# Kernel tuning notes

Measured on AMD Instinct MI355X. Metric: run time of the kernel, lower is better.

## Reference

```python
import jax, jax.numpy as jnp
import numpy as np
import math

T = 4096          # num tokens (== context_window_len)
IN_SIZE = 2048    # model dim
HEAD_SIZE = 128   # per-head dim


def setup_inputs() -> dict:
    key = jax.random.key(0)
    kx, kq, kk, kv = jax.random.split(key, 4)
    scale = 1.0 / math.sqrt(IN_SIZE)
    x = jax.random.normal(kx, (T, IN_SIZE), dtype=jnp.float32)
    # eqx.nn.Linear(in, out) weight has shape [out, in], applied as W @ x
    Wq = jax.random.normal(kq, (HEAD_SIZE, IN_SIZE), dtype=jnp.float32) * scale
    Wk = jax.random.normal(kk, (HEAD_SIZE, IN_SIZE), dtype=jnp.float32) * scale
    Wv = jax.random.normal(kv, (HEAD_SIZE, IN_SIZE), dtype=jnp.float32) * scale
    return {"x": x, "Wq": Wq, "Wk": Wk, "Wv": Wv}


def reference(x, Wq, Wk, Wv):
    # q, k, v: [T, head_size]
    q = x @ Wq.T
    k = x @ Wk.T
    v = x @ Wv.T
    # scores: [T, T]
    scores = (q @ k.T) / math.sqrt(HEAD_SIZE)
    num_toks = x.shape[0]
    # causal mask: True above the diagonal (masked out)
    causal_mask = ~jnp.tril(jnp.ones((num_toks, num_toks), dtype=bool))
    masked = jnp.where(causal_mask, -jnp.inf, scores)
    attn = jax.nn.softmax(masked, axis=-1)
    return attn @ v
```

## Files before the change

kernel.cpp:

```cpp
#include <hip/hip_runtime.h>
#include <hip/hip_bf16.h>

#define T_TOK 4096
#define D_IN  2048
#define HS    128
#define CKV   4
#define NCH   16

typedef unsigned short u16;
typedef __attribute__((ext_vector_type(8))) __bf16 bf16x8;
typedef __attribute__((ext_vector_type(4))) float f32x4;
typedef __attribute__((ext_vector_type(4))) unsigned short us4;
typedef __attribute__((ext_vector_type(8))) unsigned short us8;

#define GLOBAL_AS __attribute__((address_space(1)))
#define LDS_AS    __attribute__((address_space(3)))

__device__ __forceinline__ void async_ld16(const void* g, void* l) {
  __builtin_amdgcn_global_load_lds((GLOBAL_AS void*)(void*)g, (LDS_AS void*)l, 16, 0, 0);
}

__device__ __forceinline__ u16 f2bf(float v) {
  return __builtin_bit_cast(u16, __float2bfloat16(v));
}

__device__ __forceinline__ bool detect_f32(const u16* in, int tid, int* sflag) {
  if (tid < 64) {
    int cnt = 0;
#pragma unroll
    for (int j = 0; j < 8; j++) {
      u16 v = in[(tid * 8 + j) * 2];
      cnt += (((v >> 7) & 0xFF) >= 0xBF) ? 1 : 0;
    }
#pragma unroll
    for (int off = 1; off < 64; off <<= 1) cnt += __shfl_xor(cnt, off);
    if (tid == 0) *sflag = (cnt > 8) ? 1 : 0;
  }
  __syncthreads();
  return (*sflag != 0);
}

__global__ __launch_bounds__(256) void conv3_kernel(
    const u16* __restrict__ w0, const u16* __restrict__ w1,
    const u16* __restrict__ w2, u16* __restrict__ o0,
    u16* __restrict__ o1, u16* __restrict__ o2, int* __restrict__ flag) {
  __shared__ int sflag;
  const int mat = blockIdx.x >> 7;
  const int blk = blockIdx.x & 127;
  const u16* in = (mat == 0) ? w0 : ((mat == 1) ? w1 : w2);
  u16* out = (mat == 0) ? o0 : ((mat == 1) ? o1 : o2);
  const int tid = threadIdx.x;
  const bool isf32 = detect_f32(in, tid, &sflag);
  if (tid == 0 && mat == 0 && blk == 0) *flag = isf32 ? 1 : 0;
  const size_t base = ((size_t)blk * 256 + tid) * 8;
  if (isf32) {
    const float* f = (const float*)in;
    us4 a, b;
#pragma unroll
    for (int j = 0; j < 4; j++) a[j] = f2bf(f[base + j]);
#pragma unroll
    for (int j = 0; j < 4; j++) b[j] = f2bf(f[base + 4 + j]);
    *(us4*)(out + base) = a;
    *(us4*)(out + base + 4) = b;
  } else {
    *(us8*)(out + base) = *(const us8*)(in + base);
  }
}

__global__ __launch_bounds__(256, 2) void qkv_kernel(
    const u16* __restrict__ x, const u16* __restrict__ Wq,
    const u16* __restrict__ Wk, const u16* __restrict__ Wv,
    u16* __restrict__ Q, u16* __restrict__ K, u16* __restrict__ Vt)
{
  __shared__ __align__(16) u16 As[2][16 * 64];
  __shared__ __align__(16) u16 Bs[2][128 * 64];
  __shared__ int sflag;

  const int bid = blockIdx.x;
  const int mat = bid % 3;
  const int mtile = bid / 3;
  const u16* W = (mat == 0) ? Wq : ((mat == 1) ? Wk : Wv);
  const int tid = threadIdx.x;
  const int wv = tid >> 6, lane = tid & 63, l15 = lane & 15, quad = lane >> 4;
  const int row0 = mtile * 16;

  const bool isf32 = detect_f32(x, tid, &sflag);

  f32x4 acc[2];
#pragma unroll
  for (int i = 0; i < 2; i++) acc[i] = (f32x4)0.0f;

  const int ar = tid >> 3;
  const int ac = (tid & 7) ^ (ar & 7);

  f32x4 pa[2];
  auto loadA_f32 = [&](int k0) {
    if (tid < 128) {
      const float* xf = (const float*)x + (size_t)(row0 + ar) * D_IN + k0;
      pa[0] = *(const f32x4*)(xf + ac * 8);
      pa[1] = *(const f32x4*)(xf + ac * 8 + 4);
    }
  };
  auto writeA_f32 = [&](int buf) {
    if (tid < 128) {
      us8 c0;
#pragma unroll
      for (int j = 0; j < 4; j++) { c0[j] = f2bf(pa[0][j]); c0[4 + j] = f2bf(pa[1][j]); }
      *(us8*)((char*)As[buf] + (size_t)tid * 16) = c0;
    }
  };
  auto stageA_bf16 = [&](int k0, int buf) {
    if (wv < 2) {
      async_ld16(x + (size_t)(row0 + ar) * D_IN + k0 + ac * 8,
                 (char*)As[buf] + (size_t)wv * 1024);
    }
  };
  auto stageB = [&](int k0, int buf) {
#pragma unroll
    for (int j = 0; j < 4; j++) {
      int s = (wv * 4 + j) * 64 + lane;
      int n = s >> 3, cs = s & 7, c = cs ^ (n & 7);
      async_ld16(W + (size_t)n * D_IN + k0 + c * 8,
                 (char*)Bs[buf] + (size_t)(wv * 4 + j) * 1024);
    }
  };

  stageB(0, 0);
  if (isf32) loadA_f32(0); else stageA_bf16(0, 0);

  for (int kt = 0; kt < 32; kt++) {
    const int cur = kt & 1;
    if (isf32) writeA_f32(cur);
    __syncthreads();
    if (kt < 31) {
      stageB((kt + 1) * 64, 1 - cur);
      if (isf32) loadA_f32((kt + 1) * 64); else stageA_bf16((kt + 1) * 64, 1 - cur);
    }
#pragma unroll
    for (int kc = 0; kc < 2; kc++) {
      const int rA = l15;
      const int cl = kc * 4 + quad;
      bf16x8 a = *(const bf16x8*)((const char*)As[cur] + (rA * 8 + (cl ^ (rA & 7))) * 16);
#pragma unroll
      for (int nt = 0; nt < 2; nt++) {
        int n = wv * 32 + 16 * nt + l15;
        bf16x8 b = *(const bf16x8*)((const char*)Bs[cur] + (n * 8 + (cl ^ (n & 7))) * 16);
        acc[nt] = __builtin_amdgcn_mfma_f32_16x16x32_bf16(a, b, acc[nt], 0, 0, 0);
      }
    }
  }

  if (mat < 2) {
    u16* out = (mat == 0) ? Q : K;
#pragma unroll
    for (int nt = 0; nt < 2; nt++)
#pragma unroll
      for (int r = 0; r < 4; r++) {
        int m = row0 + quad * 4 + r;
        int n = wv * 32 + 16 * nt + l15;
        out[(size_t)m * HS + n] = f2bf(acc[nt][r]);
      }
  } else {
#pragma unroll
    for (int nt = 0; nt < 2; nt++) {
      int n = wv * 32 + 16 * nt + l15;
      int mb = row0 + quad * 4;
      us4 pk;
#pragma unroll
      for (int r = 0; r < 4; r++) pk[r] = f2bf(acc[nt][r]);
      *(us4*)(Vt + (size_t)n * T_TOK + mb) = pk;
    }
  }
}

__global__ __launch_bounds__(256, 2) void attn_split_kernel(
    const u16* __restrict__ Q, const u16* __restrict__ Kg,
    const u16* __restrict__ Vt, float* __restrict__ Opart,
    float* __restrict__ mstat, float* __restrict__ lstat)
{
  __shared__ __align__(16) u16 Ks[2][64 * 128];
  __shared__ __align__(16) u16 Vs[2][128 * 64];
  __shared__ __align__(16) u16 Ps[4 * 16 * 64];

  const int qtile = 63 - (int)blockIdx.x;
  const int ch = blockIdx.y;
  if (4 * ch > qtile) return;
  const int t0 = 4 * ch;
  const int nsteps = min(CKV, qtile + 1 - t0);
  const int q0 = qtile * 64;
  const int slot = 64 * ch - 2 * ch * (ch - 1) + (qtile - 4 * ch);

  const int tid = threadIdx.x;
  const int wv = tid >> 6, lane = tid & 63, l15 = lane & 15, quad = lane >> 4;

  bf16x8 qf[4];
#pragma unroll
  for (int kc = 0; kc < 4; kc++)
    qf[kc] = *(const bf16x8*)(Q + (size_t)(q0 + 16 * wv + l15) * HS + kc * 32 + quad * 8);

  f32x4 o[8];
#pragma unroll
  for (int i = 0; i < 8; i++) o[i] = (f32x4)0.0f;
  float mrun[4], lrun[4];
#pragma unroll
  for (int r = 0; r < 4; r++) { mrun[r] = -1e30f; lrun[r] = 0.0f; }

  const float sc = 0.12752761571239668f;

  auto stage = [&](int t, int buf) {
#pragma unroll
    for (int j = 0; j < 4; j++) {
      int s = (wv * 4 + j) * 64 + lane;
      int n = s >> 4, cs = s & 15, c = cs ^ (n & 7);
      async_ld16(Kg + (size_t)(t * 64 + n) * HS + c * 8,
                 (char*)Ks[buf] + (size_t)(wv * 4 + j) * 1024);
    }
#pragma unroll
    for (int j = 0; j < 4; j++) {
      int s = (wv * 4 + j) * 64 + lane;
      int vr = s >> 3, cs = s & 7, c = cs ^ (vr & 7);
      async_ld16(Vt + (size_t)vr * T_TOK + t * 64 + c * 8,
                 (char*)Vs[buf] + (size_t)(wv * 4 + j) * 1024);
    }
  };

  stage(t0, 0);
  for (int i = 0; i < nsteps; i++) {
    const int cur = i & 1;
    const int t = t0 + i;
    __syncthreads();
    if (i + 1 < nsteps) stage(t + 1, 1 - cur);

    f32x4 sacc[4];
#pragma unroll
    for (int nt = 0; nt < 4; nt++) sacc[nt] = (f32x4)0.0f;
    __builtin_amdgcn_s_setprio(1);
#pragma unroll
    for (int kc = 0; kc < 4; kc++) {
      const int cl = kc * 4 + quad;
#pragma unroll
      for (int nt = 0; nt < 4; nt++) {
        int n = 16 * nt + l15;
        bf16x8 b = *(const bf16x8*)((const char*)Ks[cur] + (n * 16 + (cl ^ (n & 7))) * 16);
        sacc[nt] = __builtin_amdgcn_mfma_f32_16x16x32_bf16(qf[kc], b, sacc[nt], 0, 0, 0);
      }
    }
    __builtin_amdgcn_s_setprio(0);

    float s2[4][4];
    const bool diag = (t == qtile);
#pragma unroll
    for (int nt = 0; nt < 4; nt++)
#pragma unroll
      for (int r = 0; r < 4; r++) {
        float v = sacc[nt][r] * sc;
        if (diag) {
          int qr = q0 + 16 * wv + quad * 4 + r;
          int kr = t * 64 + 16 * nt + l15;
          if (kr > qr) v = -1e30f;
        }
        s2[nt][r] = v;
      }

#pragma unroll
    for (int r = 0; r < 4; r++) {
      float tmax = fmaxf(fmaxf(s2[0][r], s2[1][r]), fmaxf(s2[2][r], s2[3][r]));
#pragma unroll
      for (int off = 1; off < 16; off <<= 1) tmax = fmaxf(tmax, __shfl_xor(tmax, off));
      if (tmax > mrun[r] + 8.0f) {
        float alpha = exp2f(mrun[r] - tmax);
#pragma unroll
        for (int c = 0; c < 8; c++) o[c][r] *= alpha;
        lrun[r] *= alpha;
        mrun[r] = tmax;
      }
    }
    float p[4][4];
#pragma unroll
    for (int r = 0; r < 4; r++) {
      float s = 0.0f;
#pragma unroll
      for (int nt = 0; nt < 4; nt++) { p[nt][r] = exp2f(s2[nt][r] - mrun[r]); s += p[nt][r]; }
#pragma unroll
      for (int off = 1; off < 16; off <<= 1) s += __shfl_xor(s, off);
      lrun[r] += s;
    }

    u16* Pw = Ps + wv * 1024;
#pragma unroll
    for (int nt = 0; nt < 4; nt++)
#pragma unroll
      for (int r = 0; r < 4; r++) {
        int row = quad * 4 + r;
        int col = nt * 16 + l15;
        int cc = col >> 3, wi = col & 7;
        Pw[(row * 8 + (cc ^ (row & 7))) * 8 + wi] = f2bf(p[nt][r]);
      }

    __builtin_amdgcn_s_setprio(1);
#pragma unroll
    for (int kc = 0; kc < 2; kc++) {
      const int cl = kc * 4 + quad;
      bf16x8 a = *(const bf16x8*)((const char*)Pw + (l15 * 8 + (cl ^ (l15 & 7))) * 16);
#pragma unroll
      for (int c = 0; c < 8; c++) {
        int vr = 16 * c + l15;
        bf16x8 b = *(const bf16x8*)((const char*)Vs[cur] + (vr * 8 + (cl ^ (vr & 7))) * 16);
        o[c] = __builtin_amdgcn_mfma_f32_16x16x32_bf16(a, b, o[c], 0, 0, 0);
      }
    }
    __builtin_amdgcn_s_setprio(0);
  }

  float* po = Opart + (size_t)slot * 64 * 128;
#pragma unroll
  for (int c = 0; c < 8; c++)
#pragma unroll
    for (int r = 0; r < 4; r++) {
      int ml = 16 * wv + quad * 4 + r;
      po[ml * 128 + 16 * c + l15] = o[c][r];
    }
  if (l15 == 0) {
#pragma unroll
    for (int r = 0; r < 4; r++) {
      int ml = 16 * wv + quad * 4 + r;
      mstat[slot * 64 + ml] = mrun[r];
      lstat[slot * 64 + ml] = lrun[r];
    }
  }
}

__global__ __launch_bounds__(256) void combine_kernel(
    const float* __restrict__ Opart, const float* __restrict__ mstat,
    const float* __restrict__ lstat, void* __restrict__ out_v,
    const int* __restrict__ dflag)
{
  const int q = blockIdx.x;
  const int cb = blockIdx.y;
  const int tid = threadIdx.x;
  const int row = tid >> 2;
  const int col = cb * 32 + (tid & 3) * 8;
  const int nch = (q + 4) / 4;
  const bool of32 = (*dflag != 0);

  float M = -1e30f;
  {
    int base = 0;
    for (int c = 0; c < nch; c++) {
      int s = base + q - 4 * c;
      M = fmaxf(M, mstat[s * 64 + row]);
      base += 64 - 4 * c;
    }
  }
  float l = 0.0f;
  float acc[8];
#pragma unroll
  for (int j = 0; j < 8; j++) acc[j] = 0.0f;
  {
    int base = 0;
    for (int c = 0; c < nch; c++) {
      int s = base + q - 4 * c;
      float w = exp2f(mstat[s * 64 + row] - M);
      l += w * lstat[s * 64 + row];
      const float* op = Opart + ((size_t)s * 64 + row) * 128 + col;
      f32x4 a = *(const f32x4*)op;
      f32x4 b = *(const f32x4*)(op + 4);
#pragma unroll
      for (int j = 0; j < 4; j++) { acc[j] += w * a[j]; acc[4 + j] += w * b[j]; }
      base += 64 - 4 * c;
    }
  }
  const float inv = 1.0f / l;
  const size_t goff = (size_t)(q * 64 + row) * HS + col;
  if (of32) {
    float* out = (float*)out_v + goff;
    f32x4 r0, r1;
#pragma unroll
    for (int j = 0; j < 4; j++) { r0[j] = acc[j] * inv; r1[j] = acc[4 + j] * inv; }
    *(f32x4*)out = r0;
    *(f32x4*)(out + 4) = r1;
  } else {
    u16* out = (u16*)out_v + goff;
    us4 r0, r1;
#pragma unroll
    for (int j = 0; j < 4; j++) { r0[j] = f2bf(acc[j] * inv); r1[j] = f2bf(acc[4 + j] * inv); }
    *(us4*)out = r0;
    *(us4*)(out + 4) = r1;
  }
}

extern "C" void kernel_launch(void* const* d_in, const int* in_sizes, int n_in,
                              void* d_out, int out_size, void* d_ws, size_t ws_size,
                              hipStream_t stream) {
  const u16* x  = (const u16*)d_in[0];
  const u16* Wq = (const u16*)d_in[1];
  const u16* Wk = (const u16*)d_in[2];
  const u16* Wv = (const u16*)d_in[3];

  float* Opart = (float*)d_ws;
  float* mstat = Opart + (size_t)544 * 64 * 128;
  float* lstat = mstat + (size_t)544 * 64;

  u16* Wqb = (u16*)(lstat + (size_t)544 * 64);
  u16* Wkb = Wqb + (size_t)HS * D_IN;
  u16* Wvb = Wkb + (size_t)HS * D_IN;
  u16* Q   = Wvb + (size_t)HS * D_IN;
  u16* K   = Q   + (size_t)T_TOK * HS;
  u16* Vt  = K   + (size_t)T_TOK * HS;
  int* flag = (int*)(Vt + (size_t)T_TOK * HS);

  conv3_kernel<<<384, 256, 0, stream>>>(Wq, Wk, Wv, Wqb, Wkb, Wvb, flag);
  qkv_kernel<<<768, 256, 0, stream>>>(x, Wqb, Wkb, Wvb, Q, K, Vt);
  attn_split_kernel<<<dim3(64, NCH), 256, 0, stream>>>(Q, K, Vt, Opart, mstat, lstat);
  combine_kernel<<<dim3(64, 4), 256, 0, stream>>>(Opart, mstat, lstat, d_out, flag);
}
```

Baseline: 142.0 us.

## Replace async LDS loads in QKV GEMM with register-staged two-ahead prefetch pipeline

Drops the global_load_lds async staging of the weight and x tiles in the QKV projection kernel. Tiles are now loaded into registers two k-steps ahead and written to double-buffered LDS, with manual lgkmcnt waits, raw s_barrier and sched_barrier fences. Occupancy in launch_bounds is also raised from 2 to 3 blocks per CU. The aim is to hide global load latency better. The cost is higher register pressure under a tighter register budget, and the global loads are no longer tracked by an explicit vmcnt wait, which relies on the compiler inserting it.

```diff
diff --git a/kernel.cpp b/kernel.cpp
--- a/kernel.cpp
+++ b/kernel.cpp
@@ -67,7 +67,7 @@
   }
 }
 
-__global__ __launch_bounds__(256, 2) void qkv_kernel(
+__global__ __launch_bounds__(256, 3) void qkv_kernel(
     const u16* __restrict__ x, const u16* __restrict__ Wq,
     const u16* __restrict__ Wk, const u16* __restrict__ Wv,
     u16* __restrict__ Q, u16* __restrict__ K, u16* __restrict__ Vt)
@@ -90,52 +90,26 @@
 #pragma unroll
   for (int i = 0; i < 2; i++) acc[i] = (f32x4)0.0f;
 
+  const u16* wp[4]; int boff[4];
+#pragma unroll
+  for (int j = 0; j < 4; j++) {
+    int s = (wv * 4 + j) * 64 + lane;
+    int n = s >> 3, c = (s & 7) ^ (n & 7);
+    wp[j] = W + (size_t)n * D_IN + c * 8;
+    boff[j] = s * 16;
+  }
   const int ar = tid >> 3;
   const int ac = (tid & 7) ^ (ar & 7);
 
-  f32x4 pa[2];
-  auto loadA_f32 = [&](int k0) {
-    if (tid < 128) {
-      const float* xf = (const float*)x + (size_t)(row0 + ar) * D_IN + k0;
-      pa[0] = *(const f32x4*)(xf + ac * 8);
-      pa[1] = *(const f32x4*)(xf + ac * 8 + 4);
-    }
+  auto loadB = [&](us8 (&d)[4], int k0) {
+#pragma unroll
+    for (int j = 0; j < 4; j++) d[j] = *(const us8*)(wp[j] + k0);
   };
-  auto writeA_f32 = [&](int buf) {
-    if (tid < 128) {
-      us8 c0;
-#pragma unroll
-      for (int j = 0; j < 4; j++) { c0[j] = f2bf(pa[0][j]); c0[4 + j] = f2bf(pa[1][j]); }
-      *(us8*)((char*)As[buf] + (size_t)tid * 16) = c0;
-    }
+  auto writeB = [&](const us8 (&s)[4], int buf) {
+#pragma unroll
+    for (int j = 0; j < 4; j++) *(us8*)((char*)Bs[buf] + boff[j]) = s[j];
   };
-  auto stageA_bf16 = [&](int k0, int buf) {
-    if (wv < 2) {
-      async_ld16(x + (size_t)(row0 + ar) * D_IN + k0 + ac * 8,
-                 (char*)As[buf] + (size_t)wv * 1024);
-    }
-  };
-  auto stageB = [&](int k0, int buf) {
-#pragma unroll
-    for (int j = 0; j < 4; j++) {
-      int s = (wv * 4 + j) * 64 + lane;
-      int n = s >> 3, cs = s & 7, c = cs ^ (n & 7);
-      async_ld16(W + (size_t)n * D_IN + k0 + c * 8,
-                 (char*)Bs[buf] + (size_t)(wv * 4 + j) * 1024);
-    }
-  };
-
-  stageB(0, 0);
-  if (isf32) loadA_f32(0); else stageA_bf16(0, 0);
-
-  for (int kt = 0; kt < 32; kt++) {
-    const int cur = kt & 1;
-    if (isf32) writeA_f32(cur);
-    __syncthreads();
-    if (kt < 31) {
-      stageB((kt + 1) * 64, 1 - cur);
-      if (isf32) loadA_f32((kt + 1) * 64); else stageA_bf16((kt + 1) * 64, 1 - cur);
-    }
+  auto compute = [&](int cur) {
 #pragma unroll
     for (int kc = 0; kc < 2; kc++) {
       const int rA = l15;
@@ -146,6 +120,83 @@
         int n = wv * 32 + 16 * nt + l15;
         bf16x8 b = *(const bf16x8*)((const char*)Bs[cur] + (n * 8 + (cl ^ (n & 7))) * 16);
         acc[nt] = __builtin_amdgcn_mfma_f32_16x16x32_bf16(a, b, acc[nt], 0, 0, 0);
+      }
+    }
+  };
+
+  if (isf32) {
+    const float* xf = (const float*)x + (size_t)(row0 + ar) * D_IN + ac * 8;
+    f32x4 a00, a01, a10, a11, aI0, aI1;
+    us8 pb0[4], pb1[4], bI[4];
+    auto loadA = [&](f32x4& d0, f32x4& d1, int k0) {
+      if (tid < 128) { d0 = *(const f32x4*)(xf + k0); d1 = *(const f32x4*)(xf + k0 + 4); }
+    };
+    auto writeA = [&](const f32x4& d0, const f32x4& d1, int buf) {
+      if (tid < 128) {
+        us8 t;
+#pragma unroll
+        for (int j = 0; j < 4; j++) { t[j] = f2bf(d0[j]); t[4 + j] = f2bf(d1[j]); }
+        *(us8*)((char*)As[buf] + (size_t)tid * 16) = t;
+      }
+    };
+
+    loadB(bI, 0);        loadA(aI0, aI1, 0);
+    loadB(pb0, 64);      loadA(a00, a01, 64);
+    loadB(pb1, 128);     loadA(a10, a11, 128);
+    writeB(bI, 0);       writeA(aI0, aI1, 0);
+    asm volatile("s_waitcnt lgkmcnt(0)" ::: "memory");
+    __builtin_amdgcn_s_barrier();
+    __builtin_amdgcn_sched_barrier(0);
+
+    for (int kt2 = 0; kt2 < 16; kt2++) {
+      const int kt = kt2 * 2;
+      writeB(pb0, 1); writeA(a00, a01, 1);
+      if (kt + 3 < 32) { loadB(pb0, (kt + 3) * 64); loadA(a00, a01, (kt + 3) * 64); }
+      compute(0);
+      asm volatile("s_waitcnt lgkmcnt(0)" ::: "memory");
+      __builtin_amdgcn_s_barrier();
+      __builtin_amdgcn_sched_barrier(0);
+      if (kt + 2 < 32) { writeB(pb1, 0); writeA(a10, a11, 0); }
+      if (kt + 4 < 32) { loadB(pb1, (kt + 4) * 64); loadA(a10, a11, (kt + 4) * 64); }
+      compute(1);
+      if (kt2 < 15) {
+        asm volatile("s_waitcnt lgkmcnt(0)" ::: "memory");
+        __builtin_amdgcn_s_barrier();
+        __builtin_amdgcn_sched_barrier(0);
+      }
+    }
+  } else {
+    const u16* xp = x + (size_t)(row0 + ar) * D_IN + ac * 8;
+    us8 qa0, qa1, qaI;
+    us8 pb0[4], pb1[4], bI[4];
+    auto loadA = [&](us8& d, int k0) { if (tid < 128) d = *(const us8*)(xp + k0); };
+    auto writeA = [&](const us8& s, int buf) {
+      if (tid < 128) *(us8*)((char*)As[buf] + (size_t)tid * 16) = s;
+    };
+
+    loadB(bI, 0);        loadA(qaI, 0);
+    loadB(pb0, 64);      loadA(qa0, 64);
+    loadB(pb1, 128);     loadA(qa1, 128);
+    writeB(bI, 0);       writeA(qaI, 0);
+    asm volatile("s_waitcnt lgkmcnt(0)" ::: "memory");
+    __builtin_amdgcn_s_barrier();
+    __builtin_amdgcn_sched_barrier(0);
+
+    for (int kt2 = 0; kt2 < 16; kt2++) {
+      const int kt = kt2 * 2;
+      writeB(pb0, 1); writeA(qa0, 1);
+      if (kt + 3 < 32) { loadB(pb0, (kt + 3) * 64); loadA(qa0, (kt + 3) * 64); }
+      compute(0);
+      asm volatile("s_waitcnt lgkmcnt(0)" ::: "memory");
+      __builtin_amdgcn_s_barrier();
+      __builtin_amdgcn_sched_barrier(0);
+      if (kt + 2 < 32) { writeB(pb1, 0); writeA(qa1, 0); }
+      if (kt + 4 < 32) { loadB(pb1, (kt + 4) * 64); loadA(qa1, (kt + 4) * 64); }
+      compute(1);
+      if (kt2 < 15) {
+        asm volatile("s_waitcnt lgkmcnt(0)" ::: "memory");
+        __builtin_amdgcn_s_barrier();
+        __builtin_amdgcn_sched_barrier(0);
       }
     }
   }
```

Result: no change. 140.4 us (-1.1%).
